# Performance work log

Measured on AMD Instinct MI355X. Metric: run time of the kernel, lower is better.

The kernel has to match this reference:

```python
import jax, jax.numpy as jnp
import numpy as np

N_DT, N_OD = 30000, 10000
D_DT, D_OD = 128, 64
H, O = 128, 64
E1, E2, EL = 500000, 300000, 200000


def _w(k, shape):
    return jax.random.normal(k, shape, jnp.float32) / np.sqrt(shape[0]).astype(np.float32)


def setup_inputs() -> dict:
    key = jax.random.key(0)
    ks = jax.random.split(key, 32)
    inp = {
        "x_dt": jax.random.normal(ks[0], (N_DT, D_DT), jnp.float32),
        "x_od": jax.random.normal(ks[1], (N_OD, D_OD), jnp.float32),
        "ei_dt": jax.random.randint(ks[2], (2, E1), 0, N_DT),
        "ei_rev_src": jax.random.randint(ks[3], (E2,), 0, N_DT),
        "ei_rev_dst": jax.random.randint(ks[4], (E2,), 0, N_OD),
        "el_src": jax.random.randint(ks[5], (EL,), 0, N_OD),
        "el_dst": jax.random.randint(ks[6], (EL,), 0, N_DT),
        # ODEncoderModel params
        "od1_wl": _w(ks[7], (D_DT, H)), "od1_wr": _w(ks[8], (D_DT, H)), "od1_b": jnp.zeros((H,), jnp.float32),
        "od2_wl": _w(ks[9], (H, H)),    "od2_wr": _w(ks[10], (D_OD, H)), "od2_b": jnp.zeros((H,), jnp.float32),
        "od3_wl": _w(ks[11], (H, H)),   "od3_wr": _w(ks[12], (H, H)),    "od3_b": jnp.zeros((H,), jnp.float32),
        "od_lw": _w(ks[13], (H, O)),    "od_lb": jnp.zeros((O,), jnp.float32),
        # DetectorTimeEncoder params
        "dt1_wl": _w(ks[14], (D_DT, H)), "dt1_wr": _w(ks[15], (D_DT, H)), "dt1_b": jnp.zeros((H,), jnp.float32),
        "dt2_wl": _w(ks[16], (H, H)),    "dt2_wr": _w(ks[17], (H, H)),    "dt2_b": jnp.zeros((H,), jnp.float32),
        "dt_lw": _w(ks[18], (H, O)),     "dt_lb": jnp.zeros((O,), jnp.float32),
        # EdgeDecoder params (hidden = out_channels = O)
        "dec_w1": _w(ks[19], (2 * O, O)), "dec_b1": jnp.zeros((O,), jnp.float32),
        "dec_w2": _w(ks[20], (O, 1)),     "dec_b2": jnp.zeros((1,), jnp.float32),
    }
    return inp


def sage(x_src, x_dst, row, col, wl, wr, b, n_dst):
    """PyG SAGEConv (aggr='mean', root_weight=True): lin_l(mean_j x_src[j]) + lin_r(x_dst)."""
    msg = jax.ops.segment_sum(x_src[row], col, num_segments=n_dst)  # [n_dst, d_src]
    cnt = jax.ops.segment_sum(jnp.ones_like(col, dtype=x_src.dtype), col, num_segments=n_dst)
    agg = msg / jnp.maximum(cnt, 1.0)[:, None]
    return agg @ wl + x_dst @ wr + b


def reference(x_dt, x_od, ei_dt, ei_rev_src, ei_rev_dst, el_src, el_dst,
              od1_wl, od1_wr, od1_b, od2_wl, od2_wr, od2_b, od3_wl, od3_wr, od3_b, od_lw, od_lb,
              dt1_wl, dt1_wr, dt1_b, dt2_wl, dt2_wr, dt2_b, dt_lw, dt_lb,
              dec_w1, dec_b1, dec_w2, dec_b2):
    r1, c1 = ei_dt[0], ei_dt[1]
    relu = jax.nn.relu
    # OD encoder: dt metapath conv, then two bipartite convs dt->od
    h = relu(sage(x_dt, x_dt, r1, c1, od1_wl, od1_wr, od1_b, N_DT))
    od = relu(sage(h, x_od, ei_rev_src, ei_rev_dst, od2_wl, od2_wr, od2_b, N_OD))
    od = relu(sage(h, od, ei_rev_src, ei_rev_dst, od3_wl, od3_wr, od3_b, N_OD))
    z_od = od @ od_lw + od_lb  # [N_OD, O]
    # DetectorTime encoder: two homogeneous convs on dt graph
    d = relu(sage(x_dt, x_dt, r1, c1, dt1_wl, dt1_wr, dt1_b, N_DT))
    d = relu(sage(d, d, r1, c1, dt2_wl, dt2_wr, dt2_b, N_DT))
    z_dt = d @ dt_lw + dt_lb  # [N_DT, O]
    # Edge decoder: gather pairs, MLP, sigmoid
    z = jnp.concatenate([z_od[el_src], z_dt[el_dst]], axis=-1)  # [EL, 2O]
    z = relu(z @ dec_w1 + dec_b1)
    return jax.nn.sigmoid(z @ dec_w2 + dec_b2).reshape(-1)  # [EL]
```

## Files before the change

kernel.cpp:

```cpp
#include <hip/hip_runtime.h>
#include <hip/hip_bf16.h>

#define NDT 30000
#define NOD 10000
#define NE1 500000
#define NE2 300000
#define NEL 200000
#define CAP_DT 64
#define CAP_OD 96

typedef unsigned short ushort_t;
typedef unsigned int uint_t;
typedef __attribute__((ext_vector_type(8))) short short8;
typedef __attribute__((ext_vector_type(4))) float f32x4;

static constexpr size_t F_BFUSE = 0;
static constexpr size_t F_ENDF  = 64;
static constexpr size_t U_XDT    = 0;
static constexpr size_t U_XOD    = U_XDT + (size_t)NDT * 128;
static constexpr size_t U_AGGX   = U_XOD + (size_t)NOD * 64;
static constexpr size_t U_H      = U_AGGX + (size_t)NDT * 128;
static constexpr size_t U_D1     = U_H + (size_t)NDT * 128;
static constexpr size_t U_AGGH   = U_D1 + (size_t)NDT * 128;
static constexpr size_t U_OD2    = U_AGGH + (size_t)NOD * 128;
static constexpr size_t U_OD3    = U_OD2 + (size_t)NOD * 128;
static constexpr size_t U_WT1A   = U_OD3 + (size_t)NOD * 128;
static constexpr size_t U_WT1B   = U_WT1A + 32768;
static constexpr size_t U_WTOD2  = U_WT1B + 32768;
static constexpr size_t U_WTOD3  = U_WTOD2 + 24576;
static constexpr size_t U_WTDT2  = U_WTOD3 + 32768;
static constexpr size_t U_WLODT  = U_WTDT2 + 32768;
static constexpr size_t U_WLDTT  = U_WLODT + 8192;
static constexpr size_t U_POD    = U_WLDTT + 8192;
static constexpr size_t U_PDT    = U_POD + (size_t)NOD * 64;
static constexpr size_t U_SRC_DT = U_PDT + (size_t)NDT * 64;
static constexpr size_t U_SRC_OD = U_SRC_DT + (size_t)NDT * CAP_DT;
static constexpr size_t U_END    = U_SRC_OD + (size_t)NOD * CAP_OD;
static constexpr size_t I_CNT_DT = 0;
static constexpr size_t I_CNT_OD = 30000;

__device__ __forceinline__ ushort_t f2bf(float f) {
    uint_t u = __float_as_uint(f);
    return (ushort_t)((u + 0x7fffu + ((u >> 16) & 1u)) >> 16);
}
__device__ __forceinline__ float bf2f(uint_t lo16) { return __uint_as_float(lo16 << 16); }

static constexpr int NB_FILL = (NE1 / 4 + 255) / 256;
static constexpr int NB_CONV = ((NDT * 128 + NOD * 64) / 4 + 255) / 256;
static constexpr int NB_WT   = (155648 + 255) / 256;
static constexpr int NB_FUSE = (16448 + 255) / 256;
static constexpr int NB_PF   = NB_FILL + NB_CONV + NB_WT + NB_FUSE;

struct PFArgs {
    const int *r1, *c1, *rev_src, *rev_dst;
    int *cnt_dt, *cnt_od;
    ushort_t *srcs_dt, *srcs_od;
    const float *x_dt, *x_od;
    ushort_t *xdt_bf, *xod_bf;
    const float *od1_wl, *od1_wr, *dt1_wl, *dt1_wr;
    const float *od2_wl, *od2_wr, *od3_wl, *od3_wr, *dt2_wl, *dt2_wr;
    ushort_t *wt1a, *wt1b, *wtod2, *wtod3, *wtdt2;
    const float *od_lw, *od_lb, *dt_lw, *dt_lb, *w1, *b1;
    ushort_t *wodt, *wdtt;
    float *bfuse;
};

__global__ __launch_bounds__(256) void prep_fill(PFArgs p) {
    int blk = blockIdx.x;
    int tid = threadIdx.x;
    if (blk < NB_FILL) {
        int b = (blk * 256 + tid) * 4;
        if (b + 3 < NE1) {
            int4 d = *(const int4*)(p.c1 + b);
            int4 s = *(const int4*)(p.r1 + b);
            int p0 = atomicAdd(&p.cnt_dt[d.x], 1);
            int p1 = atomicAdd(&p.cnt_dt[d.y], 1);
            int p2 = atomicAdd(&p.cnt_dt[d.z], 1);
            int p3 = atomicAdd(&p.cnt_dt[d.w], 1);
            if (p0 < CAP_DT) p.srcs_dt[d.x * CAP_DT + p0] = (ushort_t)s.x;
            if (p1 < CAP_DT) p.srcs_dt[d.y * CAP_DT + p1] = (ushort_t)s.y;
            if (p2 < CAP_DT) p.srcs_dt[d.z * CAP_DT + p2] = (ushort_t)s.z;
            if (p3 < CAP_DT) p.srcs_dt[d.w * CAP_DT + p3] = (ushort_t)s.w;
        } else {
            for (int i = b; i < NE1; i++) {
                int q = atomicAdd(&p.cnt_dt[p.c1[i]], 1);
                if (q < CAP_DT) p.srcs_dt[p.c1[i] * CAP_DT + q] = (ushort_t)p.r1[i];
            }
        }
        if (b + 3 < NE2) {
            int4 d = *(const int4*)(p.rev_dst + b);
            int4 s = *(const int4*)(p.rev_src + b);
            int p0 = atomicAdd(&p.cnt_od[d.x], 1);
            int p1 = atomicAdd(&p.cnt_od[d.y], 1);
            int p2 = atomicAdd(&p.cnt_od[d.z], 1);
            int p3 = atomicAdd(&p.cnt_od[d.w], 1);
            if (p0 < CAP_OD) p.srcs_od[d.x * CAP_OD + p0] = (ushort_t)s.x;
            if (p1 < CAP_OD) p.srcs_od[d.y * CAP_OD + p1] = (ushort_t)s.y;
            if (p2 < CAP_OD) p.srcs_od[d.z * CAP_OD + p2] = (ushort_t)s.z;
            if (p3 < CAP_OD) p.srcs_od[d.w * CAP_OD + p3] = (ushort_t)s.w;
        } else if (b < NE2) {
            for (int i = b; i < NE2; i++) {
                int q = atomicAdd(&p.cnt_od[p.rev_dst[i]], 1);
                if (q < CAP_OD) p.srcs_od[p.rev_dst[i] * CAP_OD + q] = (ushort_t)p.rev_src[i];
            }
        }
        return;
    }
    blk -= NB_FILL;
    if (blk < NB_CONV) {
        size_t i4 = ((size_t)blk * 256 + tid) * 4;
        const size_t n_dt = (size_t)NDT * 128, n_od = (size_t)NOD * 64;
        if (i4 < n_dt) {
            float4 v = *(const float4*)(p.x_dt + i4);
            ushort4 o = { f2bf(v.x), f2bf(v.y), f2bf(v.z), f2bf(v.w) };
            *(ushort4*)(p.xdt_bf + i4) = o;
        } else if (i4 - n_dt < n_od) {
            size_t j = i4 - n_dt;
            float4 v = *(const float4*)(p.x_od + j);
            ushort4 o = { f2bf(v.x), f2bf(v.y), f2bf(v.z), f2bf(v.w) };
            *(ushort4*)(p.xod_bf + j) = o;
        }
        return;
    }
    blk -= NB_CONV;
    if (blk < NB_WT) {
        int i = blk * 256 + tid;
        const float* wl; const float* wr; ushort_t* dst; int q, KT;
        if (i < 32768)       { q = i;          KT = 256; wl = p.od1_wl; wr = p.od1_wr; dst = p.wt1a; }
        else if (i < 65536)  { q = i - 32768;  KT = 256; wl = p.dt1_wl; wr = p.dt1_wr; dst = p.wt1b; }
        else if (i < 90112)  { q = i - 65536;  KT = 192; wl = p.od2_wl; wr = p.od2_wr; dst = p.wtod2; }
        else if (i < 122880) { q = i - 90112;  KT = 256; wl = p.od3_wl; wr = p.od3_wr; dst = p.wtod3; }
        else if (i < 155648) { q = i - 122880; KT = 256; wl = p.dt2_wl; wr = p.dt2_wr; dst = p.wtdt2; }
        else return;
        int n = q / KT, k = q - n * KT;
        float v = (k < 128) ? wl[(size_t)k * 128 + n] : wr[(size_t)(k - 128) * 128 + n];
        dst[q] = f2bf(v);
        return;
    }
    blk -= NB_WT;
    {
        int i = blk * 256 + tid;
        if (i < 8192) {
            int r = i >> 6, q = i & 63;
            float s = 0.f;
            for (int j = 0; j < 64; j++) s = fmaf(p.od_lw[r * 64 + j], p.w1[j * 64 + q], s);
            p.wodt[q * 128 + r] = f2bf(s);
        } else if (i < 16384) {
            int w = i - 8192, r = w >> 6, q = w & 63;
            float s = 0.f;
            for (int j = 0; j < 64; j++) s = fmaf(p.dt_lw[r * 64 + j], p.w1[(64 + j) * 64 + q], s);
            p.wdtt[q * 128 + r] = f2bf(s);
        } else if (i < 16448) {
            int q = i - 16384;
            float s = p.b1[q];
            for (int j = 0; j < 64; j++) {
                s = fmaf(p.od_lb[j], p.w1[j * 64 + q], s);
                s = fmaf(p.dt_lb[j], p.w1[(64 + j) * 64 + q], s);
            }
            p.bfuse[q] = s;
        }
    }
}

__global__ __launch_bounds__(64) void seg_mean_bf(const ushort_t* __restrict__ X,
                                                  const int* __restrict__ cnt,
                                                  const ushort_t* __restrict__ srcs, int cap,
                                                  ushort_t* __restrict__ out) {
    int b = blockIdx.x;
    int t = threadIdx.x;
    int deg = cnt[b];
    int n = deg < cap ? deg : cap;
    int start = b * cap;
    float lo[8] = {}, hi[8] = {};
    int j = 0;
    for (; j + 7 < n; j += 8) {
        uint_t v[8];
#pragma unroll
        for (int u = 0; u < 8; u++) {
            int s = srcs[start + j + u];
            v[u] = *(const uint_t*)&X[(size_t)s * 128 + 2 * t];
        }
#pragma unroll
        for (int u = 0; u < 8; u++) {
            lo[u] += bf2f(v[u] & 0xffff);
            hi[u] += __uint_as_float(v[u] & 0xffff0000u);
        }
    }
    for (; j < n; j++) {
        uint_t v = *(const uint_t*)&X[(size_t)srcs[start + j] * 128 + 2 * t];
        lo[0] += bf2f(v & 0xffff);
        hi[0] += __uint_as_float(v & 0xffff0000u);
    }
    float inv = deg > 0 ? 1.f / (float)deg : 0.f;
    float s0 = (((lo[0] + lo[1]) + (lo[2] + lo[3])) + ((lo[4] + lo[5]) + (lo[6] + lo[7]))) * inv;
    float s1 = (((hi[0] + hi[1]) + (hi[2] + hi[3])) + ((hi[4] + hi[5]) + (hi[6] + hi[7]))) * inv;
    *(uint_t*)&out[(size_t)b * 128 + 2 * t] = (uint_t)f2bf(s0) | ((uint_t)f2bf(s1) << 16);
}

template <bool DUAL>
__global__ __launch_bounds__(256) void sage_mfma(
    const ushort_t* __restrict__ A1, int K1,
    const ushort_t* __restrict__ A2, int K2,
    const ushort_t* __restrict__ Wta, const ushort_t* __restrict__ Wtb,
    const float* __restrict__ ba, const float* __restrict__ bb,
    ushort_t* __restrict__ outa, ushort_t* __restrict__ outb, int M) {
    __shared__ __align__(16) ushort_t As[32 * 264];
    __shared__ __align__(16) ushort_t Wsa[128 * 40];
    __shared__ __align__(16) ushort_t Wsb[DUAL ? 128 * 40 : 8];
    const int KT = K1 + K2;
    const int AST = KT + 8;
    int t = threadIdx.x;
    int lane = t & 63, wave = t >> 6;
    int quad = lane >> 4, l16 = lane & 15;
    int mtile = wave & 1, nquad = wave >> 1;
    int mb = blockIdx.x * 32;

    int c1n = 32 * (K1 >> 3);
    for (int c = t; c < c1n; c += 256) {
        int row = c / (K1 >> 3), k8 = (c % (K1 >> 3)) * 8;
        int m = mb + row; if (m >= M) m = M - 1;
        *(short8*)&As[row * AST + k8] = *(const short8*)&A1[(size_t)m * K1 + k8];
    }
    int c2n = 32 * (K2 >> 3);
    for (int c = t; c < c2n; c += 256) {
        int row = c / (K2 >> 3), k8 = (c % (K2 >> 3)) * 8;
        int m = mb + row; if (m >= M) m = M - 1;
        *(short8*)&As[row * AST + K1 + k8] = *(const short8*)&A2[(size_t)m * K2 + k8];
    }

    f32x4 acca[4] = {};
    f32x4 accb[4] = {};
    for (int kc = 0; kc < KT; kc += 32) {
        __syncthreads();
        for (int c = t; c < 512; c += 256) {
            int n = c >> 2, k8 = (c & 3) * 8;
            *(short8*)&Wsa[n * 40 + k8] = *(const short8*)&Wta[(size_t)n * KT + kc + k8];
            if (DUAL)
                *(short8*)&Wsb[n * 40 + k8] = *(const short8*)&Wtb[(size_t)n * KT + kc + k8];
        }
        __syncthreads();
        short8 af = *(const short8*)&As[(mtile * 16 + l16) * AST + kc + quad * 8];
#pragma unroll
        for (int nt = 0; nt < 4; nt++) {
            int n = (nquad * 4 + nt) * 16 + l16;
            short8 bfr = *(const short8*)&Wsa[n * 40 + quad * 8];
            acca[nt] = __builtin_amdgcn_mfma_f32_16x16x32_bf16(af, bfr, acca[nt], 0, 0, 0);
            if (DUAL) {
                short8 bfr2 = *(const short8*)&Wsb[n * 40 + quad * 8];
                accb[nt] = __builtin_amdgcn_mfma_f32_16x16x32_bf16(af, bfr2, accb[nt], 0, 0, 0);
            }
        }
    }
    int mrow = mb + mtile * 16 + quad * 4;
#pragma unroll
    for (int nt = 0; nt < 4; nt++) {
        int n = (nquad * 4 + nt) * 16 + l16;
        float bva = ba[n];
        float bvb = DUAL ? bb[n] : 0.f;
#pragma unroll
        for (int r = 0; r < 4; r++) {
            int m = mrow + r;
            if (m < M) {
                outa[(size_t)m * 128 + n] = f2bf(fmaxf(acca[nt][r] + bva, 0.f));
                if (DUAL) outb[(size_t)m * 128 + n] = f2bf(fmaxf(accb[nt][r] + bvb, 0.f));
            }
        }
    }
}

__global__ __launch_bounds__(256) void lin_mfma(const ushort_t* __restrict__ A,
                                                const ushort_t* __restrict__ Wt,
                                                ushort_t* __restrict__ out, int M) {
    __shared__ __align__(16) ushort_t As[64 * 136];
    __shared__ __align__(16) ushort_t Ws[64 * 40];
    int t = threadIdx.x;
    int lane = t & 63, wave = t >> 6;
    int quad = lane >> 4, l16 = lane & 15;
    int mb = blockIdx.x * 64;
    for (int c = t; c < 1024; c += 256) {
        int row = c >> 4, k8 = (c & 15) * 8;
        int m = mb + row; if (m >= M) m = M - 1;
        *(short8*)&As[row * 136 + k8] = *(const short8*)&A[(size_t)m * 128 + k8];
    }
    f32x4 acc[4] = {};
    for (int kc = 0; kc < 128; kc += 32) {
        __syncthreads();
        for (int c = t; c < 256; c += 256) {
            int n = c >> 2, k8 = (c & 3) * 8;
            *(short8*)&Ws[n * 40 + k8] = *(const short8*)&Wt[(size_t)n * 128 + kc + k8];
        }
        __syncthreads();
        short8 af = *(const short8*)&As[(wave * 16 + l16) * 136 + kc + quad * 8];
#pragma unroll
        for (int nt = 0; nt < 4; nt++) {
            short8 bfr = *(const short8*)&Ws[(nt * 16 + l16) * 40 + quad * 8];
            acc[nt] = __builtin_amdgcn_mfma_f32_16x16x32_bf16(af, bfr, acc[nt], 0, 0, 0);
        }
    }
    int mrow = mb + wave * 16 + quad * 4;
#pragma unroll
    for (int nt = 0; nt < 4; nt++) {
        int n = nt * 16 + l16;
#pragma unroll
        for (int r = 0; r < 4; r++) {
            int m = mrow + r;
            if (m < M) out[(size_t)m * 64 + n] = f2bf(acc[nt][r]);
        }
    }
}

__global__ __launch_bounds__(256) void decode(const ushort_t* __restrict__ P_od, const ushort_t* __restrict__ P_dt,
                                              const int* __restrict__ el_src, const int* __restrict__ el_dst,
                                              const float* __restrict__ bfuse, const float* __restrict__ w2,
                                              const float* __restrict__ b2v, float* __restrict__ out) {
    __shared__ __align__(16) float bf[64];
    __shared__ __align__(16) float w2s[64];
    int t = threadIdx.x;
    if (t < 64) { bf[t] = bfuse[t]; w2s[t] = w2[t]; }
    __syncthreads();
    int e = blockIdx.x * 256 + t;
    if (e >= NEL) return;
    const uint4* po = (const uint4*)(P_od + (size_t)el_src[e] * 64);
    const uint4* pt = (const uint4*)(P_dt + (size_t)el_dst[e] * 64);
    float acc = 0.f;
#pragma unroll
    for (int c = 0; c < 8; c++) {
        uint4 a = po[c], b = pt[c];
        const uint_t* au = (const uint_t*)&a;
        const uint_t* bu = (const uint_t*)&b;
#pragma unroll
        for (int j = 0; j < 4; j++) {
            int idx = c * 8 + j * 2;
            float lo = bf2f(au[j] & 0xffff) + bf2f(bu[j] & 0xffff) + bf[idx];
            float hi = __uint_as_float(au[j] & 0xffff0000u) + __uint_as_float(bu[j] & 0xffff0000u) + bf[idx + 1];
            acc = fmaf(fmaxf(lo, 0.f), w2s[idx], acc);
            acc = fmaf(fmaxf(hi, 0.f), w2s[idx + 1], acc);
        }
    }
    float z = acc + b2v[0];
    out[e] = 1.f / (1.f + __expf(-z));
}

extern "C" void kernel_launch(void* const* d_in, const int* in_sizes, int n_in,
                              void* d_out, int out_size, void* d_ws, size_t ws_size,
                              hipStream_t stream) {
    float* W = (float*)d_ws;
    ushort_t* U = (ushort_t*)(W + F_ENDF);
    int* I = (int*)(U + U_END);

    const float* x_dt   = (const float*)d_in[0];
    const float* x_od   = (const float*)d_in[1];
    const int* ei       = (const int*)d_in[2];
    const int* r1 = ei;
    const int* c1 = ei + NE1;
    const int* rev_src  = (const int*)d_in[3];
    const int* rev_dst  = (const int*)d_in[4];
    const int* el_src   = (const int*)d_in[5];
    const int* el_dst   = (const int*)d_in[6];
    const float* od1_wl = (const float*)d_in[7],  *od1_wr = (const float*)d_in[8],  *od1_b = (const float*)d_in[9];
    const float* od2_wl = (const float*)d_in[10], *od2_wr = (const float*)d_in[11], *od2_b = (const float*)d_in[12];
    const float* od3_wl = (const float*)d_in[13], *od3_wr = (const float*)d_in[14], *od3_b = (const float*)d_in[15];
    const float* od_lw  = (const float*)d_in[16], *od_lb  = (const float*)d_in[17];
    const float* dt1_wl = (const float*)d_in[18], *dt1_wr = (const float*)d_in[19], *dt1_b = (const float*)d_in[20];
    const float* dt2_wl = (const float*)d_in[21], *dt2_wr = (const float*)d_in[22], *dt2_b = (const float*)d_in[23];
    const float* dt_lw  = (const float*)d_in[24], *dt_lb  = (const float*)d_in[25];
    const float* dec_w1 = (const float*)d_in[26], *dec_b1 = (const float*)d_in[27];
    const float* dec_w2 = (const float*)d_in[28], *dec_b2 = (const float*)d_in[29];

    hipMemsetAsync(I + I_CNT_DT, 0, (NDT + NOD) * sizeof(int), stream);

    PFArgs p;
    p.r1 = r1; p.c1 = c1; p.rev_src = rev_src; p.rev_dst = rev_dst;
    p.cnt_dt = I + I_CNT_DT; p.cnt_od = I + I_CNT_OD;
    p.srcs_dt = U + U_SRC_DT; p.srcs_od = U + U_SRC_OD;
    p.x_dt = x_dt; p.x_od = x_od;
    p.xdt_bf = U + U_XDT; p.xod_bf = U + U_XOD;
    p.od1_wl = od1_wl; p.od1_wr = od1_wr; p.dt1_wl = dt1_wl; p.dt1_wr = dt1_wr;
    p.od2_wl = od2_wl; p.od2_wr = od2_wr; p.od3_wl = od3_wl; p.od3_wr = od3_wr;
    p.dt2_wl = dt2_wl; p.dt2_wr = dt2_wr;
    p.wt1a = U + U_WT1A; p.wt1b = U + U_WT1B; p.wtod2 = U + U_WTOD2;
    p.wtod3 = U + U_WTOD3; p.wtdt2 = U + U_WTDT2;
    p.od_lw = od_lw; p.od_lb = od_lb; p.dt_lw = dt_lw; p.dt_lb = dt_lb;
    p.w1 = dec_w1; p.b1 = dec_b1;
    p.wodt = U + U_WLODT; p.wdtt = U + U_WLDTT;
    p.bfuse = W + F_BFUSE;
    prep_fill<<<NB_PF, 256, 0, stream>>>(p);

    seg_mean_bf<<<NDT, 64, 0, stream>>>(U + U_XDT, I + I_CNT_DT, U + U_SRC_DT, CAP_DT, U + U_AGGX);
    sage_mfma<true><<<(NDT + 31) / 32, 256, 0, stream>>>(U + U_AGGX, 128, U + U_XDT, 128,
                                                         U + U_WT1A, U + U_WT1B, od1_b, dt1_b,
                                                         U + U_H, U + U_D1, NDT);
    seg_mean_bf<<<NOD, 64, 0, stream>>>(U + U_H, I + I_CNT_OD, U + U_SRC_OD, CAP_OD, U + U_AGGH);
    sage_mfma<false><<<(NOD + 31) / 32, 256, 0, stream>>>(U + U_AGGH, 128, U + U_XOD, 64,
                                                          U + U_WTOD2, nullptr, od2_b, nullptr,
                                                          U + U_OD2, nullptr, NOD);
    sage_mfma<false><<<(NOD + 31) / 32, 256, 0, stream>>>(U + U_AGGH, 128, U + U_OD2, 128,
                                                          U + U_WTOD3, nullptr, od3_b, nullptr,
                                                          U + U_OD3, nullptr, NOD);
    seg_mean_bf<<<NDT, 64, 0, stream>>>(U + U_D1, I + I_CNT_DT, U + U_SRC_DT, CAP_DT, U + U_AGGX);
    sage_mfma<false><<<(NDT + 31) / 32, 256, 0, stream>>>(U + U_AGGX, 128, U + U_D1, 128,
                                                          U + U_WTDT2, nullptr, dt2_b, nullptr,
                                                          U + U_H, nullptr, NDT);
    lin_mfma<<<(NOD + 63) / 64, 256, 0, stream>>>(U + U_OD3, U + U_WLODT, U + U_POD, NOD);
    lin_mfma<<<(NDT + 63) / 64, 256, 0, stream>>>(U + U_H, U + U_WLDTT, U + U_PDT, NDT);
    decode<<<(NEL + 255) / 256, 256, 0, stream>>>(U + U_POD, U + U_PDT, el_src, el_dst,
                                                  W + F_BFUSE, dec_w2, dec_b2, (float*)d_out);
}
```

Measured before the change: 295.3 us.

## Batch independent DT and OD stages into shared kernel launches

Independent work from the two encoders now runs in combined grids, with blocks split between jobs by block index. The DT segment mean and OD segment mean share one launch, as do the DT layer-2 and OD layer-2 SAGE GEMMs and the two final linear projections. This cuts the number of launches and lets the small OD grids fill the device alongside the larger DT grids instead of running alone. The cost is a runtime job-selection branch and job parameters passed by struct, which may cost registers or stop some compile-time specialization.

Result: faster. 279.5 us, median of 2 (-5.4%).

```diff
diff --git a/kernel.cpp b/kernel.cpp
--- a/kernel.cpp
+++ b/kernel.cpp
@@ -162,12 +162,10 @@
     }
 }
 
-__global__ __launch_bounds__(64) void seg_mean_bf(const ushort_t* __restrict__ X,
-                                                  const int* __restrict__ cnt,
-                                                  const ushort_t* __restrict__ srcs, int cap,
-                                                  ushort_t* __restrict__ out) {
-    int b = blockIdx.x;
-    int t = threadIdx.x;
+__device__ __forceinline__ void seg_mean_body(const ushort_t* __restrict__ X,
+                                              const int* __restrict__ cnt,
+                                              const ushort_t* __restrict__ srcs, int cap,
+                                              ushort_t* __restrict__ out, int b, int t) {
     int deg = cnt[b];
     int n = deg < cap ? deg : cap;
     int start = b * cap;
@@ -195,6 +193,22 @@
     float s0 = (((lo[0] + lo[1]) + (lo[2] + lo[3])) + ((lo[4] + lo[5]) + (lo[6] + lo[7]))) * inv;
     float s1 = (((hi[0] + hi[1]) + (hi[2] + hi[3])) + ((hi[4] + hi[5]) + (hi[6] + hi[7]))) * inv;
     *(uint_t*)&out[(size_t)b * 128 + 2 * t] = (uint_t)f2bf(s0) | ((uint_t)f2bf(s1) << 16);
+}
+
+__global__ __launch_bounds__(64) void seg_mean_bf(const ushort_t* __restrict__ X,
+                                                  const int* __restrict__ cnt,
+                                                  const ushort_t* __restrict__ srcs, int cap,
+                                                  ushort_t* __restrict__ out) {
+    seg_mean_body(X, cnt, srcs, cap, out, blockIdx.x, threadIdx.x);
+}
+
+__global__ __launch_bounds__(64) void seg_mean2(const ushort_t* Xa, const int* cnta, const ushort_t* srca,
+                                                int capa, ushort_t* outa, int Na,
+                                                const ushort_t* Xb, const int* cntb, const ushort_t* srcb,
+                                                int capb, ushort_t* outb) {
+    int b = blockIdx.x;
+    if (b < Na) seg_mean_body(Xa, cnta, srca, capa, outa, b, threadIdx.x);
+    else        seg_mean_body(Xb, cntb, srcb, capb, outb, b - Na, threadIdx.x);
 }
 
 template <bool DUAL>
@@ -227,7 +241,6 @@
         int m = mb + row; if (m >= M) m = M - 1;
         *(short8*)&As[row * AST + K1 + k8] = *(const short8*)&A2[(size_t)m * K2 + k8];
     }
-
     f32x4 acca[4] = {};
     f32x4 accb[4] = {};
     for (int kc = 0; kc < KT; kc += 32) {
@@ -268,26 +281,94 @@
     }
 }
 
-__global__ __launch_bounds__(256) void lin_mfma(const ushort_t* __restrict__ A,
-                                                const ushort_t* __restrict__ Wt,
-                                                ushort_t* __restrict__ out, int M) {
-    __shared__ __align__(16) ushort_t As[64 * 136];
-    __shared__ __align__(16) ushort_t Ws[64 * 40];
+struct SageJob {
+    const ushort_t *A1, *A2;
+    int K1, K2;
+    const ushort_t *Wt;
+    const float *bias;
+    ushort_t *out;
+    int M;
+};
+
+__global__ __launch_bounds__(256) void sage_two(SageJob ja, int nb_a, SageJob jb) {
+    __shared__ __align__(16) ushort_t As[32 * 264];
+    __shared__ __align__(16) ushort_t Wsa[128 * 40];
+    SageJob j;
+    int blk;
+    if (blockIdx.x < nb_a) { j = ja; blk = blockIdx.x; }
+    else                   { j = jb; blk = blockIdx.x - nb_a; }
+    const int KT = j.K1 + j.K2;
+    const int AST = KT + 8;
     int t = threadIdx.x;
     int lane = t & 63, wave = t >> 6;
     int quad = lane >> 4, l16 = lane & 15;
-    int mb = blockIdx.x * 64;
+    int mtile = wave & 1, nquad = wave >> 1;
+    int mb = blk * 32;
+
+    int c1n = 32 * (j.K1 >> 3);
+    for (int c = t; c < c1n; c += 256) {
+        int row = c / (j.K1 >> 3), k8 = (c % (j.K1 >> 3)) * 8;
+        int m = mb + row; if (m >= j.M) m = j.M - 1;
+        *(short8*)&As[row * AST + k8] = *(const short8*)&j.A1[(size_t)m * j.K1 + k8];
+    }
+    int c2n = 32 * (j.K2 >> 3);
+    for (int c = t; c < c2n; c += 256) {
+        int row = c / (j.K2 >> 3), k8 = (c % (j.K2 >> 3)) * 8;
+        int m = mb + row; if (m >= j.M) m = j.M - 1;
+        *(short8*)&As[row * AST + j.K1 + k8] = *(const short8*)&j.A2[(size_t)m * j.K2 + k8];
+    }
+    f32x4 acc[4] = {};
+    for (int kc = 0; kc < KT; kc += 32) {
+        __syncthreads();
+        for (int c = t; c < 512; c += 256) {
+            int n = c >> 2, k8 = (c & 3) * 8;
+            *(short8*)&Wsa[n * 40 + k8] = *(const short8*)&j.Wt[(size_t)n * KT + kc + k8];
+        }
+        __syncthreads();
+        short8 af = *(const short8*)&As[(mtile * 16 + l16) * AST + kc + quad * 8];
+#pragma unroll
+        for (int nt = 0; nt < 4; nt++) {
+            int n = (nquad * 4 + nt) * 16 + l16;
+            short8 bfr = *(const short8*)&Wsa[n * 40 + quad * 8];
+            acc[nt] = __builtin_amdgcn_mfma_f32_16x16x32_bf16(af, bfr, acc[nt], 0, 0, 0);
+        }
+    }
+    int mrow = mb + mtile * 16 + quad * 4;
+#pragma unroll
+    for (int nt = 0; nt < 4; nt++) {
+        int n = (nquad * 4 + nt) * 16 + l16;
+        float bv = j.bias[n];
+#pragma unroll
+        for (int r = 0; r < 4; r++) {
+            int m = mrow + r;
+            if (m < j.M) j.out[(size_t)m * 128 + n] = f2bf(fmaxf(acc[nt][r] + bv, 0.f));
+        }
+    }
+}
+
+struct LinJob {
+    const ushort_t *A, *Wt;
+    ushort_t *out;
+    int M;
+};
+
+__device__ __forceinline__ void lin_body(const LinJob& j, int blk, int t) {
+    __shared__ __align__(16) ushort_t As[64 * 136];
+    __shared__ __align__(16) ushort_t Ws[64 * 40];
+    int lane = t & 63, wave = t >> 6;
+    int quad = lane >> 4, l16 = lane & 15;
+    int mb = blk * 64;
     for (int c = t; c < 1024; c += 256) {
         int row = c >> 4, k8 = (c & 15) * 8;
-        int m = mb + row; if (m >= M) m = M - 1;
-        *(short8*)&As[row * 136 + k8] = *(const short8*)&A[(size_t)m * 128 + k8];
+        int m = mb + row; if (m >= j.M) m = j.M - 1;
+        *(short8*)&As[row * 136 + k8] = *(const short8*)&j.A[(size_t)m * 128 + k8];
     }
     f32x4 acc[4] = {};
     for (int kc = 0; kc < 128; kc += 32) {
         __syncthreads();
         for (int c = t; c < 256; c += 256) {
             int n = c >> 2, k8 = (c & 3) * 8;
-            *(short8*)&Ws[n * 40 + k8] = *(const short8*)&Wt[(size_t)n * 128 + kc + k8];
+            *(short8*)&Ws[n * 40 + k8] = *(const short8*)&j.Wt[(size_t)n * 128 + kc + k8];
         }
         __syncthreads();
         short8 af = *(const short8*)&As[(wave * 16 + l16) * 136 + kc + quad * 8];
@@ -304,9 +385,14 @@
 #pragma unroll
         for (int r = 0; r < 4; r++) {
             int m = mrow + r;
-            if (m < M) out[(size_t)m * 64 + n] = f2bf(acc[nt][r]);
-        }
-    }
+            if (m < j.M) j.out[(size_t)m * 64 + n] = f2bf(acc[nt][r]);
+        }
+    }
+}
+
+__global__ __launch_bounds__(256) void lin_two(LinJob ja, int nb_a, LinJob jb) {
+    if (blockIdx.x < nb_a) lin_body(ja, blockIdx.x, threadIdx.x);
+    else                   lin_body(jb, blockIdx.x - nb_a, threadIdx.x);
 }
 
 __global__ __launch_bounds__(256) void decode(const ushort_t* __restrict__ P_od, const ushort_t* __restrict__ P_dt,
@@ -390,19 +476,25 @@
     sage_mfma<true><<<(NDT + 31) / 32, 256, 0, stream>>>(U + U_AGGX, 128, U + U_XDT, 128,
                                                          U + U_WT1A, U + U_WT1B, od1_b, dt1_b,
                                                          U + U_H, U + U_D1, NDT);
-    seg_mean_bf<<<NOD, 64, 0, stream>>>(U + U_H, I + I_CNT_OD, U + U_SRC_OD, CAP_OD, U + U_AGGH);
-    sage_mfma<false><<<(NOD + 31) / 32, 256, 0, stream>>>(U + U_AGGH, 128, U + U_XOD, 64,
-                                                          U + U_WTOD2, nullptr, od2_b, nullptr,
-                                                          U + U_OD2, nullptr, NOD);
+    seg_mean2<<<NDT + NOD, 64, 0, stream>>>(U + U_D1, I + I_CNT_DT, U + U_SRC_DT, CAP_DT, U + U_AGGX, NDT,
+                                            U + U_H, I + I_CNT_OD, U + U_SRC_OD, CAP_OD, U + U_AGGH);
+    {
+        SageJob jd2 = { U + U_AGGX, U + U_D1, 128, 128, U + U_WTDT2, dt2_b, U + U_H, NDT };
+        SageJob jod2 = { U + U_AGGH, U + U_XOD, 128, 64, U + U_WTOD2, od2_b, U + U_OD2, NOD };
+        int nb_d2 = (NDT + 31) / 32;
+        int nb_od2 = (NOD + 31) / 32;
+        sage_two<<<nb_d2 + nb_od2, 256, 0, stream>>>(jd2, nb_d2, jod2);
+    }
     sage_mfma<false><<<(NOD + 31) / 32, 256, 0, stream>>>(U + U_AGGH, 128, U + U_OD2, 128,
                                                           U + U_WTOD3, nullptr, od3_b, nullptr,
                                                           U + U_OD3, nullptr, NOD);
-    seg_mean_bf<<<NDT, 64, 0, stream>>>(U + U_D1, I + I_CNT_DT, U + U_SRC_DT, CAP_DT, U + U_AGGX);
-    sage_mfma<false><<<(NDT + 31) / 32, 256, 0, stream>>>(U + U_AGGX, 128, U + U_D1, 128,
-                                                          U + U_WTDT2, nullptr, dt2_b, nullptr,
-                                                          U + U_H, nullptr, NDT);
-    lin_mfma<<<(NOD + 63) / 64, 256, 0, stream>>>(U + U_OD3, U + U_WLODT, U + U_POD, NOD);
-    lin_mfma<<<(NDT + 63) / 64, 256, 0, stream>>>(U + U_H, U + U_WLDTT, U + U_PDT, NDT);
+    {
+        LinJob jdt = { U + U_H, U + U_WLDTT, U + U_PDT, NDT };
+        LinJob jod = { U + U_OD3, U + U_WLODT, U + U_POD, NOD };
+        int nb_dt = (NDT + 63) / 64;
+        int nb_od = (NOD + 63) / 64;
+        lin_two<<<nb_dt + nb_od, 256, 0, stream>>>(jdt, nb_dt, jod);
+    }
     decode<<<(NEL + 255) / 256, 256, 0, stream>>>(U + U_POD, U + U_PDT, el_src, el_dst,
                                                   W + F_BFUSE, dec_w2, dec_b2, (float*)d_out);
 }
```
